# Performance work log

Measured on AMD Instinct MI355X. Metric: run time of the kernel, lower is better.

## Reference

```python
import jax, jax.numpy as jnp
import numpy as np

B, N, C, H, EXP = 8, 1024, 256, 8, 4
D = C // H
F = int(C * EXP * 2 / 3)  # 682, GLU hidden size
EPS = 1e-3  # keras LayerNormalization default


def layer_norm(x, g, b):
    m = jnp.mean(x, axis=-1, keepdims=True)
    v = jnp.mean(jnp.square(x - m), axis=-1, keepdims=True)
    return (x - m) * jax.lax.rsqrt(v + EPS) * g + b


def setup_inputs() -> dict:
    key = jax.random.key(0)
    ks = jax.random.split(key, 16)
    inputs = jax.random.normal(ks[0], (B, N, C), jnp.float32)
    # ragged padding mask: random valid lengths per batch element
    lengths = jax.random.randint(ks[1], (B,), N // 2, N + 1)
    valid = jnp.arange(N)[None, :] < lengths[:, None]          # [B,N]
    mask = valid[:, :, None] & valid[:, None, :]               # [B,N,N]
    interaction = jax.random.normal(ks[2], (B, N, N, H), jnp.float32)
    s = lambda k, sh, fan: jax.random.normal(k, sh, jnp.float32) / np.sqrt(fan)
    return {
        "inputs": inputs, "mask": mask, "interaction": interaction,
        "Wqkv": s(ks[3], (C, 3 * C), C), "bqkv": jnp.zeros((3 * C,), jnp.float32),
        "Wt1": s(ks[4], (H, H), H), "bt1": jnp.zeros((H,), jnp.float32),
        "Wt2": s(ks[5], (H, H), H), "bt2": jnp.zeros((H,), jnp.float32),
        "Wout": s(ks[6], (C, C), C), "bout": jnp.zeros((C,), jnp.float32),
        "ln1_g": jnp.ones((C,), jnp.float32), "ln1_b": jnp.zeros((C,), jnp.float32),
        "ln2_g": jnp.ones((C,), jnp.float32), "ln2_b": jnp.zeros((C,), jnp.float32),
        "gamma1": jnp.full((C,), 1e-5, jnp.float32),
        "gamma2": jnp.full((C,), 1e-5, jnp.float32),
        "W_wide": s(ks[7], (C, F), C), "W_gate": s(ks[8], (C, F), C),
        "W_down": s(ks[9], (F, C), F),
        "lnf_g": jnp.ones((F,), jnp.float32), "lnf_b": jnp.zeros((F,), jnp.float32),
    }


def reference(inputs, mask, interaction, Wqkv, bqkv, Wt1, bt1, Wt2, bt2,
              Wout, bout, ln1_g, ln1_b, ln2_g, ln2_b, gamma1, gamma2,
              W_wide, W_gate, W_down, lnf_g, lnf_b):
    # --- pre-norm talking-heads self-attention ---
    h = layer_norm(inputs, ln1_g, ln1_b)
    qkv = (h @ Wqkv + bqkv).reshape(B, N, 3, H, D)
    qkv = jnp.transpose(qkv, (2, 0, 3, 1, 4))                 # [3,B,H,N,D]
    q, k, v = qkv[0], qkv[1], qkv[2]
    scores = jnp.einsum('bhnd,bhmd->bhnm', q, k) / np.sqrt(D) # [B,H,N,N]
    # talking heads 1 (pre-softmax head mixing, with bias)
    scores = jnp.einsum('bhnm,hg->bgnm', scores, Wt1) + bt1[None, :, None, None]
    scores = scores + jnp.transpose(interaction, (0, 3, 1, 2))
    # keras Softmax(mask): add -1e9 to masked positions
    scores = jnp.where(mask[:, None, :, :], scores, scores - 1e9)
    attn = jax.nn.softmax(scores, axis=-1)                    # pure attention
    # talking heads 2 (post-softmax head mixing)
    attn2 = jnp.einsum('bhnm,hg->bgnm', attn, Wt2) + bt2[None, :, None, None]
    out = jnp.einsum('bhnm,bhmd->bhnd', attn2, v)
    out = jnp.transpose(out, (0, 2, 1, 3)).reshape(B, N, C)
    out = out @ Wout + bout
    x = inputs + gamma1 * out                                  # LayerScale residual
    # --- GLU FFN with inner LayerNorm ---
    h2 = layer_norm(x, ln2_g, ln2_b)
    f = jax.nn.gelu(h2 @ W_wide, approximate=False) * (h2 @ W_gate)
    f = layer_norm(f, lnf_g, lnf_b)
    f = f @ W_down
    x = x + gamma2 * f
    return x
```

## Files before the change

kernel.cpp:

```cpp
#include <hip/hip_runtime.h>
#include <hip/hip_bf16.h>
#include <math.h>

#define B_ 8
#define N_ 1024
#define C_ 256
#define H_ 8
#define D_ 32
#define F_ 682
#define FP_ 704
#define EPS_ 1e-3f

typedef const __hip_bfloat16* bf16cp;
typedef __hip_bfloat16 bf16;
typedef __attribute__((ext_vector_type(8))) short short8;
typedef __attribute__((ext_vector_type(4))) float f32x4;

__device__ __forceinline__ float b2f(bf16 v){ return __bfloat162float(v); }
__device__ __forceinline__ float us2f(unsigned int u){ return __uint_as_float(u << 16); }
__device__ __forceinline__ unsigned short f2bu(float f){
  unsigned int u = __float_as_uint(f);
  return (unsigned short)((u + 0x7FFFu + ((u >> 16) & 1u)) >> 16);
}

__device__ __forceinline__ float ldf(const void* p, size_t i, int bf){
  return bf ? b2f(((bf16cp)p)[i]) : ((const float*)p)[i];
}

struct Ptrs { const void* p[22]; };

__global__ __launch_bounds__(64) void k_sniffp(Ptrs ptrs, int* flags){
  int i = blockIdx.x;
  int lane = threadIdx.x;
  if (i == 1){ if (lane == 0) flags[1] = 0; return; }
  const int sizes[22] = {2097152, 8388608, 8388608, 196608, 768, 64, 8, 64, 8,
                         65536, 256, 256, 256, 256, 256, 256, 256,
                         174592, 174592, 174592, 682, 682};
  const unsigned short* u = (const unsigned short*)ptrs.p[i];
  int nu = sizes[i] < 64 ? sizes[i] : 64;
  unsigned short x = 0;
  if (lane < nu) x = u[lane];
  int predB = 0;
  if (lane < nu){
    float vb = us2f((unsigned int)x);
    float ab = fabsf(vb);
    predB = (!(vb == 0.0f) && (!(ab <= 1e3f) || ab < 1e-30f || vb != vb)) ? 1 : 0;
  }
  unsigned long long mB = __ballot(predB);
  int badB = __popcll(mB);
  unsigned long long mEven = __ballot(lane < nu && (lane & 1) == 0 && x != 0);
  unsigned long long mOdd  = __ballot(lane < nu && (lane & 1) == 1 && x != 0);
  int evenAllZero = (mEven == 0ull);
  int oddAny = (mOdd != 0ull);
  unsigned short xa = (unsigned short)__shfl((int)x, (lane * 2) & 63);
  unsigned short xb = (unsigned short)__shfl((int)x, (lane * 2 + 1) & 63);
  int predF = 0;
  if (lane < (nu >> 1)){
    unsigned int w = ((unsigned int)xa) | (((unsigned int)xb) << 16);
    float vf = __uint_as_float(w);
    float af = fabsf(vf);
    predF = (!(vf == 0.0f) && (!(af <= 1e3f) || af < 1e-30f || vf != vf)) ? 1 : 0;
  }
  int badF = __popcll(__ballot(predF));
  if (lane == 0){
    int bf;
    if (badB > badF) bf = 0;
    else if (badF > badB) bf = 1;
    else bf = (evenAllZero && oddAny) ? 0 : 1;
    flags[i] = bf;
  }
}

__global__ __launch_bounds__(256) void k_lengths(const unsigned char* mask, int* lengths){
  __shared__ int red[256];
  int b = blockIdx.x, t = threadIdx.x;
  unsigned char c0 = mask[0], c1 = mask[1];
  int mode;
  if (c0 == 0x80u) mode = 2;
  else if (c0 == 0u) mode = 3;
  else mode = (c1 != 0u) ? 0 : 1;
  int cnt = 0;
  for (int n = t; n < N_; n += 256){
    size_t idx = ((size_t)b*N_ + n)*N_ + n;
    int v;
    if (mode == 0)      v = (mask[idx] != 0);
    else if (mode == 1) v = (((const int*)mask)[idx] != 0);
    else if (mode == 2) v = (((const unsigned short*)mask)[idx] != 0);
    else                v = (((const float*)mask)[idx] != 0.0f);
    cnt += v;
  }
  red[t] = cnt; __syncthreads();
  for (int s = 128; s > 0; s >>= 1){ if (t < s) red[t] += red[t+s]; __syncthreads(); }
  if (t == 0) lengths[b] = red[0];
}

__global__ __launch_bounds__(256) void k_ln(const void* in, const int* flags, int in_mode,
                                            const void* g, int gi, const void* bia, int bi,
                                            void* out, int out_bf16, int Clen, int stride){
  __shared__ float red[256];
  int fin = (in_mode >= 0) ? flags[in_mode] : (in_mode == -2 ? 1 : 0);
  int fg = flags[gi], fb = flags[bi];
  int row = blockIdx.x, t = threadIdx.x;
  size_t base = (size_t)row * stride;
  float xs[3];
  int nv = (Clen + 255) >> 8;
  float s = 0.f;
  for (int i = 0; i < nv; i++){
    int c = t + (i << 8);
    float v = 0.f;
    if (c < Clen) v = ldf(in, base+c, fin);
    xs[i] = v; s += v;
  }
  red[t] = s; __syncthreads();
  for (int st = 128; st > 0; st >>= 1){ if (t < st) red[t] += red[t+st]; __syncthreads(); }
  float mean = red[0] / (float)Clen; __syncthreads();
  float s2 = 0.f;
  for (int i = 0; i < nv; i++){
    int c = t + (i << 8);
    if (c < Clen){ float d = xs[i] - mean; s2 += d*d; }
  }
  red[t] = s2; __syncthreads();
  for (int st = 128; st > 0; st >>= 1){ if (t < st) red[t] += red[t+st]; __syncthreads(); }
  float rstd = rsqrtf(red[0] / (float)Clen + EPS_);
  for (int i = 0; i < nv; i++){
    int c = t + (i << 8);
    if (c < Clen){
      float v = (xs[i]-mean)*rstd*ldf(g,c,fg) + ldf(bia,c,fb);
      if (out_bf16) ((bf16*)out)[base+c] = __float2bfloat16(v);
      else          ((float*)out)[base+c] = v;
    }
  }
}

__global__ __launch_bounds__(256) void k_prepw(Ptrs ptrs, const int* flags,
                                               unsigned short* wqkvT, unsigned short* woutT,
                                               unsigned short* wwideT, unsigned short* wgateT,
                                               unsigned short* wdownT){
  __shared__ unsigned short tile[32][33];
  int which = blockIdx.y;
  const void* src; unsigned short* dst; int f, Ksrc, Nsrc, Np, Kp;
  switch (which){
    case 0:  src = ptrs.p[3];  f = flags[3];  Ksrc = 256; Nsrc = 768; Np = 768; Kp = 256; dst = wqkvT; break;
    case 1:  src = ptrs.p[9];  f = flags[9];  Ksrc = 256; Nsrc = 256; Np = 256; Kp = 256; dst = woutT; break;
    case 2:  src = ptrs.p[17]; f = flags[17]; Ksrc = 256; Nsrc = F_;  Np = FP_; Kp = 256; dst = wwideT; break;
    case 3:  src = ptrs.p[18]; f = flags[18]; Ksrc = 256; Nsrc = F_;  Np = FP_; Kp = 256; dst = wgateT; break;
    default: src = ptrs.p[19]; f = flags[19]; Ksrc = F_;  Nsrc = 256; Np = 256; Kp = FP_; dst = wdownT; break;
  }
  int tilesN = (Np + 31) >> 5, tilesK = (Kp + 31) >> 5;
  int tid = blockIdx.x;
  if (tid >= tilesN * tilesK) return;
  int tn = tid % tilesN, tk = tid / tilesN;
  int n0 = tn << 5, k0 = tk << 5;
  int tx = threadIdx.x & 31, ty = threadIdx.x >> 5;
  #pragma unroll
  for (int i = 0; i < 4; i++){
    int k = k0 + ty + i*8, n = n0 + tx;
    float v = (k < Ksrc && n < Nsrc) ? ldf(src, (size_t)k*Nsrc + n, f) : 0.f;
    tile[ty + i*8][tx] = f2bu(v);
  }
  __syncthreads();
  #pragma unroll
  for (int i = 0; i < 4; i++){
    int n = n0 + ty + i*8, k = k0 + tx;
    if (n < Np && k < Kp) dst[(size_t)n*Kp + k] = tile[tx][ty + i*8];
  }
}

__global__ __launch_bounds__(256) void k_vt(const bf16* vb, unsigned short* vt){
  __shared__ unsigned short tile[32][34];
  int mt = blockIdx.x, bg = blockIdx.y;
  int tx = threadIdx.x & 31, ty = threadIdx.x >> 5;
  const unsigned short* vus = (const unsigned short*)vb;
  #pragma unroll
  for (int i = 0; i < 4; i++){
    int m = mt*32 + ty + i*8;
    tile[ty + i*8][tx] = vus[((size_t)bg*N_ + m)*D_ + tx];
  }
  __syncthreads();
  #pragma unroll
  for (int i = 0; i < 4; i++){
    int d = ty + i*8;
    vt[((size_t)bg*D_ + d)*N_ + mt*32 + tx] = tile[tx][d];
  }
}

__device__ __forceinline__ void gemm128_core(const unsigned short* A, const unsigned short* BT,
                                             int K, int m0, int n0,
                                             unsigned short* As, unsigned short* Bs,
                                             f32x4 (&acc)[4][4]){
  int t = threadIdx.x;
  int lane = t & 63, w = t >> 6, wr = w >> 1, wc = w & 1;
  int cl = lane & 15, cq = lane >> 4;
  int r0 = t >> 2, o0 = (t & 3) << 3;
  const unsigned short* Ap = A + (size_t)(m0 + r0) * K + o0;
  const unsigned short* Bp = BT + (size_t)(n0 + r0) * K + o0;
  for (int k0 = 0; k0 < K; k0 += 32){
    short8 a0 = *(const short8*)(Ap + k0);
    short8 a1 = *(const short8*)(Ap + (size_t)64*K + k0);
    short8 b0 = *(const short8*)(Bp + k0);
    short8 b1 = *(const short8*)(Bp + (size_t)64*K + k0);
    __syncthreads();
    *(short8*)(As + r0*40 + o0)      = a0;
    *(short8*)(As + (r0+64)*40 + o0) = a1;
    *(short8*)(Bs + r0*40 + o0)      = b0;
    *(short8*)(Bs + (r0+64)*40 + o0) = b1;
    __syncthreads();
    short8 af[4], bfr[4];
    #pragma unroll
    for (int i = 0; i < 4; i++){
      af[i]  = *(const short8*)(As + (wr*64 + i*16 + cl)*40 + cq*8);
      bfr[i] = *(const short8*)(Bs + (wc*64 + i*16 + cl)*40 + cq*8);
    }
    #pragma unroll
    for (int i = 0; i < 4; i++)
      #pragma unroll
      for (int j = 0; j < 4; j++)
        acc[i][j] = __builtin_amdgcn_mfma_f32_16x16x32_bf16(af[i], bfr[j], acc[i][j], 0, 0, 0);
  }
}

__global__ __launch_bounds__(256) void k_qkv(const bf16* Abuf, const unsigned short* WT,
                                             const void* bias, const int* flags,
                                             bf16* qb, bf16* kb, bf16* vb){
  __shared__ unsigned short As[128*40], Bs[128*40];
  int fb = flags[4];
  int m0 = blockIdx.x * 128, n0 = blockIdx.y * 128;
  f32x4 acc[4][4];
  #pragma unroll
  for (int i = 0; i < 4; i++)
    #pragma unroll
    for (int j = 0; j < 4; j++){ f32x4 z = {0.f,0.f,0.f,0.f}; acc[i][j] = z; }
  gemm128_core((const unsigned short*)Abuf, WT, C_, m0, n0, As, Bs, acc);
  int t = threadIdx.x, lane = t & 63, w = t >> 6, wr = w >> 1, wc = w & 1;
  int cl = lane & 15, cq = lane >> 4;
  #pragma unroll
  for (int j = 0; j < 4; j++){
    int n = n0 + wc*64 + j*16 + cl;
    float bv = ldf(bias, n, fb);
    int three = n >> 8, hh = (n >> 5) & 7, d = n & 31;
    bf16* dst = (three == 0) ? qb : ((three == 1) ? kb : vb);
    #pragma unroll
    for (int i = 0; i < 4; i++){
      #pragma unroll
      for (int r = 0; r < 4; r++){
        int m = m0 + wr*64 + i*16 + cq*4 + r;
        int bb = m >> 10, nn = m & 1023;
        dst[(((size_t)bb*H_ + hh)*N_ + nn)*D_ + d] = __float2bfloat16(acc[i][j][r] + bv);
      }
    }
  }
}

__global__ __launch_bounds__(256) void k_outproj(const bf16* Abuf, const unsigned short* WT,
                                                 const void* bias, const void* inputs,
                                                 const void* gamma1, const int* flags, float* xout){
  __shared__ unsigned short As[128*40], Bs[128*40];
  int fb = flags[10], fin = flags[0], fg = flags[15];
  int m0 = blockIdx.x * 128, n0 = blockIdx.y * 128;
  f32x4 acc[4][4];
  #pragma unroll
  for (int i = 0; i < 4; i++)
    #pragma unroll
    for (int j = 0; j < 4; j++){ f32x4 z = {0.f,0.f,0.f,0.f}; acc[i][j] = z; }
  gemm128_core((const unsigned short*)Abuf, WT, C_, m0, n0, As, Bs, acc);
  int t = threadIdx.x, lane = t & 63, w = t >> 6, wr = w >> 1, wc = w & 1;
  int cl = lane & 15, cq = lane >> 4;
  #pragma unroll
  for (int j = 0; j < 4; j++){
    int n = n0 + wc*64 + j*16 + cl;
    float bv = ldf(bias, n, fb);
    float gv = ldf(gamma1, n, fg);
    #pragma unroll
    for (int i = 0; i < 4; i++){
      #pragma unroll
      for (int r = 0; r < 4; r++){
        int m = m0 + wr*64 + i*16 + cq*4 + r;
        size_t idx = (size_t)m*C_ + n;
        xout[idx] = ldf(inputs, idx, fin) + gv * (acc[i][j][r] + bv);
      }
    }
  }
}

__device__ __forceinline__ float gelu_exact(float x){
  return 0.5f * x * (1.0f + erff(x * 0.70710678118654752f));
}

__global__ __launch_bounds__(256) void k_ffn1(const bf16* Abuf, const unsigned short* WwT,
                                              const unsigned short* WgT, bf16* fout){
  __shared__ unsigned short As[128*40], Bw[64*40], Bg[64*40];
  int m0 = blockIdx.x * 128, n0 = blockIdx.y * 64;
  int t = threadIdx.x, lane = t & 63, w = t >> 6, wr = w >> 1, wc = w & 1;
  int cl = lane & 15, cq = lane >> 4;
  int r0 = t >> 2, o0 = (t & 3) << 3;
  const unsigned short* A = (const unsigned short*)Abuf;
  f32x4 acc1[4][2], acc2[4][2];
  #pragma unroll
  for (int i = 0; i < 4; i++)
    #pragma unroll
    for (int j = 0; j < 2; j++){ f32x4 z = {0.f,0.f,0.f,0.f}; acc1[i][j] = z; acc2[i][j] = z; }
  const unsigned short* Ap = A + (size_t)(m0 + r0) * C_ + o0;
  const unsigned short* Bwp = WwT + (size_t)(n0 + r0) * C_ + o0;
  const unsigned short* Bgp = WgT + (size_t)(n0 + r0) * C_ + o0;
  for (int k0 = 0; k0 < C_; k0 += 32){
    short8 a0 = *(const short8*)(Ap + k0);
    short8 a1 = *(const short8*)(Ap + (size_t)64*C_ + k0);
    short8 b0, c0;
    if (r0 < 64){
      b0 = *(const short8*)(Bwp + k0);
      c0 = *(const short8*)(Bgp + k0);
    }
    __syncthreads();
    *(short8*)(As + r0*40 + o0)      = a0;
    *(short8*)(As + (r0+64)*40 + o0) = a1;
    if (r0 < 64){
      *(short8*)(Bw + r0*40 + o0) = b0;
      *(short8*)(Bg + r0*40 + o0) = c0;
    }
    __syncthreads();
    short8 af[4], bfr[2], cfr[2];
    #pragma unroll
    for (int i = 0; i < 4; i++)
      af[i] = *(const short8*)(As + (wr*64 + i*16 + cl)*40 + cq*8);
    #pragma unroll
    for (int j = 0; j < 2; j++){
      bfr[j] = *(const short8*)(Bw + (wc*32 + j*16 + cl)*40 + cq*8);
      cfr[j] = *(const short8*)(Bg + (wc*32 + j*16 + cl)*40 + cq*8);
    }
    #pragma unroll
    for (int i = 0; i < 4; i++)
      #pragma unroll
      for (int j = 0; j < 2; j++){
        acc1[i][j] = __builtin_amdgcn_mfma_f32_16x16x32_bf16(af[i], bfr[j], acc1[i][j], 0, 0, 0);
        acc2[i][j] = __builtin_amdgcn_mfma_f32_16x16x32_bf16(af[i], cfr[j], acc2[i][j], 0, 0, 0);
      }
  }
  #pragma unroll
  for (int j = 0; j < 2; j++){
    int n = n0 + wc*32 + j*16 + cl;
    #pragma unroll
    for (int i = 0; i < 4; i++){
      #pragma unroll
      for (int r = 0; r < 4; r++){
        int m = m0 + wr*64 + i*16 + cq*4 + r;
        float v = (n < F_) ? gelu_exact(acc1[i][j][r]) * acc2[i][j][r] : 0.f;
        fout[(size_t)m*FP_ + n] = __float2bfloat16(v);
      }
    }
  }
}

__global__ __launch_bounds__(256) void k_down(const bf16* Abuf, const unsigned short* WT,
                                              const float* xbuf, const void* gamma2,
                                              const int* flags, void* out){
  __shared__ unsigned short As[128*40], Bs[128*40];
  int fg = flags[16], fo = flags[0];
  int m0 = blockIdx.x * 128, n0 = blockIdx.y * 128;
  f32x4 acc[4][4];
  #pragma unroll
  for (int i = 0; i < 4; i++)
    #pragma unroll
    for (int j = 0; j < 4; j++){ f32x4 z = {0.f,0.f,0.f,0.f}; acc[i][j] = z; }
  gemm128_core((const unsigned short*)Abuf, WT, FP_, m0, n0, As, Bs, acc);
  int t = threadIdx.x, lane = t & 63, w = t >> 6, wr = w >> 1, wc = w & 1;
  int cl = lane & 15, cq = lane >> 4;
  #pragma unroll
  for (int j = 0; j < 4; j++){
    int n = n0 + wc*64 + j*16 + cl;
    float gv = ldf(gamma2, n, fg);
    #pragma unroll
    for (int i = 0; i < 4; i++){
      #pragma unroll
      for (int r = 0; r < 4; r++){
        int m = m0 + wr*64 + i*16 + cq*4 + r;
        size_t idx = (size_t)m*C_ + n;
        float val = xbuf[idx] + gv * acc[i][j][r];
        if (fo) ((bf16*)out)[idx] = __float2bfloat16(val);
        else    ((float*)out)[idx] = val;
      }
    }
  }
}

__global__ __launch_bounds__(256) void k_vsum(const bf16* vb, float* vsum){
  __shared__ float red[8][32];
  int bg = blockIdx.x;
  int t = threadIdx.x;
  int d = t & 31, mg = t >> 5;
  float s = 0.f;
  for (int m = mg*128; m < mg*128 + 128; m++)
    s += b2f(vb[((size_t)bg*N_ + m)*D_ + d]);
  red[mg][d] = s; __syncthreads();
  if (t < 32){
    float a = 0.f;
    #pragma unroll
    for (int i = 0; i < 8; i++) a += red[i][t];
    vsum[(size_t)bg*D_ + t] = a;
  }
}

__global__ __launch_bounds__(256) void k_passA(const bf16* qb, const bf16* kb,
                                               const void* Wt1, const void* bt1, const void* inter,
                                               const int* flags, const int* lengths,
                                               unsigned short* P, float* Lp){
  __shared__ float w1s[64], b1v[8];
  __shared__ unsigned short ps[4][8][640];
  __shared__ float swL[4][8][16];
  int fw1 = flags[5], fb1 = flags[6], fint = flags[2];
  int t = threadIdx.x;
  int ntile = blockIdx.x, b = blockIdx.y, z = blockIdx.z;
  int n0 = ntile * 16;
  int len = lengths[b];
  if (t < 64) w1s[t] = ldf(Wt1, t, fw1) * 0.17677669529663687f;
  if (t < 8)  b1v[t] = ldf(bt1, t, fb1);
  __syncthreads();
  int lane = t & 63, w = t >> 6;
  int c = lane & 15, q = lane >> 4;
  const unsigned short* qus = (const unsigned short*)qb;
  const unsigned short* kus = (const unsigned short*)kb;
  short8 qfrag[8];
  #pragma unroll
  for (int h = 0; h < 8; h++)
    qfrag[h] = *(const short8*)(qus + (((size_t)b*8 + h)*N_ + n0 + c)*D_ + q*8);
  float Lacc[8][4];
  #pragma unroll
  for (int g = 0; g < 8; g++)
    #pragma unroll
    for (int r = 0; r < 4; r++) Lacc[g][r] = 0.f;

  for (int ci = 0; ci < 4; ci++){
    int m0c = z*512 + w*128 + ci*32;
    #pragma unroll
    for (int mt = 0; mt < 2; mt++){
      int m0t = m0c + mt*16;
      f32x4 sfr[8];
      #pragma unroll
      for (int h = 0; h < 8; h++){
        short8 kf = *(const short8*)(kus + (((size_t)b*8 + h)*N_ + m0t + c)*D_ + q*8);
        f32x4 zz = {0.f,0.f,0.f,0.f};
        sfr[h] = __builtin_amdgcn_mfma_f32_16x16x32_bf16(qfrag[h], kf, zz, 0, 0, 0);
      }
      int m_g = m0t + c;
      bool mok = (m_g < len);
      #pragma unroll
      for (int r = 0; r < 4; r++){
        int n_l = q*4 + r, n_gg = n0 + n_l;
        size_t i8 = ((size_t)b*N_ + n_gg)*N_ + m_g;
        float ifl[8];
        if (fint){
          uint4 iv = *(const uint4*)((const unsigned short*)inter + i8*8);
          ifl[0]=us2f(iv.x&0xffffu); ifl[1]=us2f(iv.x>>16);
          ifl[2]=us2f(iv.y&0xffffu); ifl[3]=us2f(iv.y>>16);
          ifl[4]=us2f(iv.z&0xffffu); ifl[5]=us2f(iv.z>>16);
          ifl[6]=us2f(iv.w&0xffffu); ifl[7]=us2f(iv.w>>16);
        } else {
          const float* fp = (const float*)inter + i8*8;
          #pragma unroll
          for (int g = 0; g < 8; g++) ifl[g] = fp[g];
        }
        bool ok = (n_gg >= len) || mok;
        #pragma unroll
        for (int g = 0; g < 8; g++){
          float v = b1v[g] + ifl[g];
          #pragma unroll
          for (int h = 0; h < 8; h++) v += sfr[h][r] * w1s[h*8 + g];
          float e = ok ? __expf(v) : 0.f;
          Lacc[g][r] += e;
          ps[w][g][n_l*40 + mt*16 + c] = f2bu(e);
        }
      }
    }
    #pragma unroll
    for (int it = 0; it < 8; it++){
      int row = it*16 + (lane >> 2);
      int g = row >> 4, n = row & 15, chunk = lane & 3;
      short8 pv = *(const short8*)&ps[w][g][n*40 + chunk*8];
      *(short8*)(P + (((size_t)b*8 + g)*N_ + n0 + n)*N_ + m0c + chunk*8) = pv;
    }
  }
  #pragma unroll
  for (int g = 0; g < 8; g++)
    #pragma unroll
    for (int r = 0; r < 4; r++){
      float v = Lacc[g][r];
      v += __shfl_xor(v, 1); v += __shfl_xor(v, 2);
      v += __shfl_xor(v, 4); v += __shfl_xor(v, 8);
      Lacc[g][r] = v;
    }
  if (c == 0){
    #pragma unroll
    for (int g = 0; g < 8; g++)
      #pragma unroll
      for (int r = 0; r < 4; r++) swL[w][g][q*4 + r] = Lacc[g][r];
  }
  __syncthreads();
  if (t < 128){
    int g = t >> 4, nl = t & 15;
    float Lf = swL[0][g][nl] + swL[1][g][nl] + swL[2][g][nl] + swL[3][g][nl];
    Lp[(((size_t)b*8 + g)*N_ + n0 + nl)*2 + z] = Lf;
  }
}

__global__ __launch_bounds__(256) void k_passB(const unsigned short* P, const unsigned short* vt,
                                               const void* Wt2, const void* bt2,
                                               const int* flags, const float* Lp,
                                               const float* vsum, bf16* aobuf){
  __shared__ float w2s[64], b2v[8];
  __shared__ float rLs[8][16];
  __shared__ float vsumS[4][32];
  __shared__ float osum[4][528];
  int fw2 = flags[7], fb2 = flags[8];
  int t = threadIdx.x;
  int ntile = blockIdx.x, b = blockIdx.y, zh = blockIdx.z;
  int n0 = ntile * 16;
  if (t < 64) w2s[t] = ldf(Wt2, t, fw2);
  if (t < 8)  b2v[t] = ldf(bt2, t, fb2);
  if (t < 128){
    int g = t >> 4, nl = t & 15;
    const float* lp = Lp + (((size_t)b*8 + g)*N_ + n0 + nl)*2;
    rLs[g][nl] = 1.0f / (lp[0] + lp[1]);
  }
  if (t >= 128 && t < 256){
    int e = t - 128;
    int g2 = e >> 5, d = e & 31;
    vsumS[g2][d] = vsum[((size_t)b*8 + zh*4 + g2)*D_ + d];
  }
  __syncthreads();
  int lane = t & 63, w = t >> 6;
  int c = lane & 15, q = lane >> 4;
  float rL[8];
  #pragma unroll
  for (int g = 0; g < 8; g++) rL[g] = rLs[g][c];
  float w2r[8][4];
  #pragma unroll
  for (int g = 0; g < 8; g++)
    #pragma unroll
    for (int j = 0; j < 4; j++) w2r[g][j] = w2s[g*8 + zh*4 + j];
  f32x4 acc[4][2];
  #pragma unroll
  for (int gg = 0; gg < 4; gg++){ f32x4 z = {0.f,0.f,0.f,0.f}; acc[gg][0] = z; acc[gg][1] = z; }

  for (int ci = 0; ci < 8; ci++){
    int m0c = w*256 + ci*32;
    short8 pf[8];
    #pragma unroll
    for (int g = 0; g < 8; g++)
      pf[g] = *(const short8*)(P + (((size_t)b*8 + g)*N_ + n0 + c)*N_ + m0c + q*8);
    float a2[4][8];
    #pragma unroll
    for (int gg = 0; gg < 4; gg++)
      #pragma unroll
      for (int j = 0; j < 8; j++) a2[gg][j] = 0.f;
    #pragma unroll
    for (int j = 0; j < 8; j++){
      #pragma unroll
      for (int g = 0; g < 8; g++){
        float png = us2f((unsigned int)(unsigned short)pf[g][j]) * rL[g];
        a2[0][j] += png * w2r[g][0];
        a2[1][j] += png * w2r[g][1];
        a2[2][j] += png * w2r[g][2];
        a2[3][j] += png * w2r[g][3];
      }
    }
    #pragma unroll
    for (int gg = 0; gg < 4; gg++){
      short8 af;
      #pragma unroll
      for (int j = 0; j < 8; j++) af[j] = (short)f2bu(a2[gg][j]);
      int ggg = zh*4 + gg;
      short8 bf0 = *(const short8*)(vt + (((size_t)b*8 + ggg)*D_ + c)*N_ + m0c + q*8);
      short8 bf1 = *(const short8*)(vt + (((size_t)b*8 + ggg)*D_ + 16 + c)*N_ + m0c + q*8);
      acc[gg][0] = __builtin_amdgcn_mfma_f32_16x16x32_bf16(af, bf0, acc[gg][0], 0, 0, 0);
      acc[gg][1] = __builtin_amdgcn_mfma_f32_16x16x32_bf16(af, bf1, acc[gg][1], 0, 0, 0);
    }
  }
  for (int gg = 0; gg < 4; gg++){
    #pragma unroll
    for (int dt = 0; dt < 2; dt++)
      #pragma unroll
      for (int r = 0; r < 4; r++)
        osum[w][(q*4 + r)*33 + dt*16 + c] = acc[gg][dt][r];
    __syncthreads();
    int ggg = zh*4 + gg;
    #pragma unroll
    for (int e = t; e < 512; e += 256){
      int nl = e >> 5, d = e & 31;
      float val = osum[0][nl*33 + d] + osum[1][nl*33 + d]
                + osum[2][nl*33 + d] + osum[3][nl*33 + d]
                + b2v[ggg] * vsumS[gg][d];
      aobuf[((size_t)b*N_ + n0 + nl)*C_ + ggg*D_ + d] = __float2bfloat16(val);
    }
    __syncthreads();
  }
}

extern "C" void kernel_launch(void* const* d_in, const int* in_sizes, int n_in,
                              void* d_out, int out_size, void* d_ws, size_t ws_size,
                              hipStream_t stream) {
  Ptrs ptrs;
  for (int i = 0; i < 22; i++) ptrs.p[i] = d_in[i];
  const unsigned char* mask = (const unsigned char*)d_in[1];

  char* ws = (char*)d_ws;
  size_t o = 0;
  size_t o_flags = o; o += 256;
  size_t o_len   = o; o += 256;
  size_t o_L     = o; o += (size_t)B_*H_*N_*2*4;
  size_t o_vsum  = o; o += (size_t)B_*H_*D_*4;
  size_t o_h     = o; o += (size_t)B_*N_*C_*2;
  size_t o_q     = o; o += (size_t)B_*N_*C_*2;
  size_t o_k     = o; o += (size_t)B_*N_*C_*2;
  size_t o_v     = o; o += (size_t)B_*N_*C_*2;
  size_t o_vt    = o; o += (size_t)B_*N_*C_*2;
  size_t o_ao    = o; o += (size_t)B_*N_*C_*2;
  size_t o_x     = o; o += (size_t)B_*N_*C_*4;
  size_t o_f     = o; o += (size_t)B_*N_*FP_*2;
  size_t o_wq    = o; o += (size_t)768*256*2;
  size_t o_wo    = o; o += (size_t)256*256*2;
  size_t o_ww    = o; o += (size_t)FP_*256*2;
  size_t o_wg    = o; o += (size_t)FP_*256*2;
  size_t o_wd    = o; o += (size_t)256*FP_*2;
  size_t o_P     = o; o += (size_t)B_*H_*N_*N_*2;

  int*    flags   = (int*)(ws + o_flags);
  int*    lengths = (int*)(ws + o_len);
  float*  Lp      = (float*)(ws + o_L);
  float*  vsum    = (float*)(ws + o_vsum);
  bf16*   hbuf    = (bf16*)(ws + o_h);
  bf16*   qbuf    = (bf16*)(ws + o_q);
  bf16*   kbuf    = (bf16*)(ws + o_k);
  bf16*   vbuf    = (bf16*)(ws + o_v);
  unsigned short* vtbuf = (unsigned short*)(ws + o_vt);
  bf16*   aobuf   = (bf16*)(ws + o_ao);
  float*  xbuf    = (float*)(ws + o_x);
  bf16*   fbuf    = (bf16*)(ws + o_f);
  unsigned short* wqkvT  = (unsigned short*)(ws + o_wq);
  unsigned short* woutT  = (unsigned short*)(ws + o_wo);
  unsigned short* wwideT = (unsigned short*)(ws + o_ww);
  unsigned short* wgateT = (unsigned short*)(ws + o_wg);
  unsigned short* wdownT = (unsigned short*)(ws + o_wd);
  unsigned short* Pbuf   = (unsigned short*)(ws + o_P);

  k_sniffp<<<22, 64, 0, stream>>>(ptrs, flags);
  k_prepw<<<dim3(192, 5), 256, 0, stream>>>(ptrs, flags, wqkvT, woutT, wwideT, wgateT, wdownT);
  k_lengths<<<8, 256, 0, stream>>>(mask, lengths);
  k_ln<<<B_*N_, 256, 0, stream>>>(d_in[0], flags, 0, d_in[11], 11, d_in[12], 12, hbuf, 1, C_, C_);
  k_qkv<<<dim3(64, 6), 256, 0, stream>>>(hbuf, wqkvT, d_in[4], flags, qbuf, kbuf, vbuf);
  k_vt<<<dim3(32, 64), 256, 0, stream>>>(vbuf, vtbuf);
  k_vsum<<<64, 256, 0, stream>>>(vbuf, vsum);
  k_passA<<<dim3(64, 8, 2), 256, 0, stream>>>(qbuf, kbuf, d_in[5], d_in[6], d_in[2],
                                              flags, lengths, Pbuf, Lp);
  k_passB<<<dim3(64, 8, 2), 256, 0, stream>>>(Pbuf, vtbuf, d_in[7], d_in[8],
                                              flags, Lp, vsum, aobuf);
  k_outproj<<<dim3(64, 2), 256, 0, stream>>>(aobuf, woutT, d_in[10], d_in[0], d_in[15], flags, xbuf);
  k_ln<<<B_*N_, 256, 0, stream>>>(xbuf, flags, -1, d_in[13], 13, d_in[14], 14, hbuf, 1, C_, C_);
  k_ffn1<<<dim3(64, 11), 256, 0, stream>>>(hbuf, wwideT, wgateT, fbuf);
  k_ln<<<B_*N_, 256, 0, stream>>>(fbuf, flags, -2, d_in[20], 20, d_in[21], 21, fbuf, 1, F_, FP_);
  k_down<<<dim3(64, 2), 256, 0, stream>>>(fbuf, wdownT, xbuf, d_in[16], flags, d_out);
}
```

Baseline: 851.1 us.

## Fold talking-heads pre-softmax mix into Q so MFMA computes mixed scores directly

Adds a kernel that premultiplies Q by the Wt1 head-mixing weights, producing one mixed Q per output head over the full 256-wide channel. passA can then compute mixed scores with a K=256 MFMA contraction instead of eight per-head MFMAs followed by a scalar 8x8 mix per element. Q and K are now stored flat, Q tiles are staged in XOR-swizzled shared memory, the z-split over keys is removed, and P is written directly without the shared staging buffer. passB loads P in two groups of four heads to cut register pressure. The cost is an extra kernel and a 32 MB qmix buffer. The P stores become scattered 2-byte writes and the grid has half as many blocks.

```diff
diff --git a/kernel.cpp b/kernel.cpp
--- a/kernel.cpp
+++ b/kernel.cpp
@@ -221,7 +221,7 @@
 
 __global__ __launch_bounds__(256) void k_qkv(const bf16* Abuf, const unsigned short* WT,
                                              const void* bias, const int* flags,
-                                             bf16* qb, bf16* kb, bf16* vb){
+                                             bf16* qflat, bf16* kflat, bf16* vb){
   __shared__ unsigned short As[128*40], Bs[128*40];
   int fb = flags[4];
   int m0 = blockIdx.x * 128, n0 = blockIdx.y * 128;
@@ -238,16 +238,41 @@
     int n = n0 + wc*64 + j*16 + cl;
     float bv = ldf(bias, n, fb);
     int three = n >> 8, hh = (n >> 5) & 7, d = n & 31;
-    bf16* dst = (three == 0) ? qb : ((three == 1) ? kb : vb);
     #pragma unroll
     for (int i = 0; i < 4; i++){
       #pragma unroll
       for (int r = 0; r < 4; r++){
         int m = m0 + wr*64 + i*16 + cq*4 + r;
         int bb = m >> 10, nn = m & 1023;
-        dst[(((size_t)bb*H_ + hh)*N_ + nn)*D_ + d] = __float2bfloat16(acc[i][j][r] + bv);
-      }
-    }
+        bf16 val = __float2bfloat16(acc[i][j][r] + bv);
+        if (three == 0)      qflat[((size_t)bb*N_ + nn)*C_ + hh*32 + d] = val;
+        else if (three == 1) kflat[((size_t)bb*N_ + nn)*C_ + hh*32 + d] = val;
+        else                 vb[(((size_t)bb*H_ + hh)*N_ + nn)*D_ + d] = val;
+      }
+    }
+  }
+}
+
+__global__ __launch_bounds__(256) void k_qmix(const bf16* qflat, const void* Wt1, const int* flags,
+                                              unsigned short* qmix){
+  __shared__ float w1s[64];
+  int t = threadIdx.x;
+  if (t < 64) w1s[t] = ldf(Wt1, t, flags[5]) * 0.17677669529663687f;
+  __syncthreads();
+  int ntile = blockIdx.x, b = blockIdx.y;
+  const unsigned short* qus = (const unsigned short*)qflat;
+  for (int it = 0; it < 16; it++){
+    int flat = it*256 + t;
+    int g = flat >> 9, nl = (flat >> 5) & 15, c8 = flat & 31;
+    int h = c8 >> 2;
+    int nn = ntile*16 + nl;
+    short8 qv = *(const short8*)(qus + ((size_t)b*N_ + nn)*C_ + c8*8);
+    float wv = w1s[h*8 + g];
+    short8 ov;
+    #pragma unroll
+    for (int j = 0; j < 8; j++)
+      ov[j] = (short)f2bu(us2f((unsigned int)(unsigned short)qv[j]) * wv);
+    *(short8*)(qmix + (((size_t)b*8 + g)*N_ + nn)*C_ + c8*8) = ov;
   }
 }
 
@@ -399,83 +424,83 @@
   }
 }
 
-__global__ __launch_bounds__(256) void k_passA(const bf16* qb, const bf16* kb,
-                                               const void* Wt1, const void* bt1, const void* inter,
+__global__ __launch_bounds__(256) void k_passA(const unsigned short* qmix, const unsigned short* kflat,
+                                               const void* bt1, const void* inter,
                                                const int* flags, const int* lengths,
                                                unsigned short* P, float* Lp){
-  __shared__ float w1s[64], b1v[8];
-  __shared__ unsigned short ps[4][8][640];
+  __shared__ unsigned short qls[128*256];
   __shared__ float swL[4][8][16];
-  int fw1 = flags[5], fb1 = flags[6], fint = flags[2];
+  int fb1 = flags[6], fint = flags[2];
   int t = threadIdx.x;
-  int ntile = blockIdx.x, b = blockIdx.y, z = blockIdx.z;
+  int ntile = blockIdx.x, b = blockIdx.y;
   int n0 = ntile * 16;
   int len = lengths[b];
-  if (t < 64) w1s[t] = ldf(Wt1, t, fw1) * 0.17677669529663687f;
-  if (t < 8)  b1v[t] = ldf(bt1, t, fb1);
+  float b1r[8];
+  #pragma unroll
+  for (int g = 0; g < 8; g++) b1r[g] = ldf(bt1, g, fb1);
+  for (int it = 0; it < 16; it++){
+    int flat = it*256 + t;
+    int row = flat >> 5, ch = flat & 31;
+    int g = row >> 4, nl = row & 15;
+    short8 v = *(const short8*)(qmix + (((size_t)b*8 + g)*N_ + n0 + nl)*C_ + ch*8);
+    unsigned int off = (unsigned)row*512u + (unsigned)ch*16u;
+    off ^= (unsigned)((row & 7) << 4);
+    *(short8*)((char*)qls + off) = v;
+  }
   __syncthreads();
   int lane = t & 63, w = t >> 6;
   int c = lane & 15, q = lane >> 4;
-  const unsigned short* qus = (const unsigned short*)qb;
-  const unsigned short* kus = (const unsigned short*)kb;
-  short8 qfrag[8];
-  #pragma unroll
-  for (int h = 0; h < 8; h++)
-    qfrag[h] = *(const short8*)(qus + (((size_t)b*8 + h)*N_ + n0 + c)*D_ + q*8);
   float Lacc[8][4];
   #pragma unroll
   for (int g = 0; g < 8; g++)
     #pragma unroll
     for (int r = 0; r < 4; r++) Lacc[g][r] = 0.f;
 
-  for (int ci = 0; ci < 4; ci++){
-    int m0c = z*512 + w*128 + ci*32;
-    #pragma unroll
-    for (int mt = 0; mt < 2; mt++){
-      int m0t = m0c + mt*16;
-      f32x4 sfr[8];
-      #pragma unroll
-      for (int h = 0; h < 8; h++){
-        short8 kf = *(const short8*)(kus + (((size_t)b*8 + h)*N_ + m0t + c)*D_ + q*8);
-        f32x4 zz = {0.f,0.f,0.f,0.f};
-        sfr[h] = __builtin_amdgcn_mfma_f32_16x16x32_bf16(qfrag[h], kf, zz, 0, 0, 0);
-      }
-      int m_g = m0t + c;
-      bool mok = (m_g < len);
-      #pragma unroll
-      for (int r = 0; r < 4; r++){
-        int n_l = q*4 + r, n_gg = n0 + n_l;
-        size_t i8 = ((size_t)b*N_ + n_gg)*N_ + m_g;
-        float ifl[8];
-        if (fint){
-          uint4 iv = *(const uint4*)((const unsigned short*)inter + i8*8);
-          ifl[0]=us2f(iv.x&0xffffu); ifl[1]=us2f(iv.x>>16);
-          ifl[2]=us2f(iv.y&0xffffu); ifl[3]=us2f(iv.y>>16);
-          ifl[4]=us2f(iv.z&0xffffu); ifl[5]=us2f(iv.z>>16);
-          ifl[6]=us2f(iv.w&0xffffu); ifl[7]=us2f(iv.w>>16);
-        } else {
-          const float* fp = (const float*)inter + i8*8;
-          #pragma unroll
-          for (int g = 0; g < 8; g++) ifl[g] = fp[g];
-        }
-        bool ok = (n_gg >= len) || mok;
-        #pragma unroll
-        for (int g = 0; g < 8; g++){
-          float v = b1v[g] + ifl[g];
-          #pragma unroll
-          for (int h = 0; h < 8; h++) v += sfr[h][r] * w1s[h*8 + g];
-          float e = ok ? __expf(v) : 0.f;
-          Lacc[g][r] += e;
-          ps[w][g][n_l*40 + mt*16 + c] = f2bu(e);
-        }
-      }
-    }
-    #pragma unroll
-    for (int it = 0; it < 8; it++){
-      int row = it*16 + (lane >> 2);
-      int g = row >> 4, n = row & 15, chunk = lane & 3;
-      short8 pv = *(const short8*)&ps[w][g][n*40 + chunk*8];
-      *(short8*)(P + (((size_t)b*8 + g)*N_ + n0 + n)*N_ + m0c + chunk*8) = pv;
+  for (int mt = 0; mt < 16; mt++){
+    int m0t = w*256 + mt*16;
+    f32x4 acc[8];
+    #pragma unroll
+    for (int g = 0; g < 8; g++){ f32x4 z = {0.f,0.f,0.f,0.f}; acc[g] = z; }
+    const unsigned short* kfp = kflat + ((size_t)b*N_ + m0t + c)*C_ + q*8;
+    #pragma unroll
+    for (int kc = 0; kc < 8; kc++){
+      short8 kf = *(const short8*)(kfp + kc*32);
+      #pragma unroll
+      for (int g = 0; g < 8; g++){
+        unsigned int off = ((unsigned)(g*16 + c)*512u + (unsigned)(kc*64 + q*16)) ^ (unsigned)((c & 7) << 4);
+        short8 qm = *(const short8*)((const char*)qls + off);
+        acc[g] = __builtin_amdgcn_mfma_f32_16x16x32_bf16(qm, kf, acc[g], 0, 0, 0);
+      }
+    }
+    int m_g = m0t + c;
+    bool mok = (m_g < len);
+    #pragma unroll
+    for (int r = 0; r < 4; r++){
+      int n_gg = n0 + q*4 + r;
+      size_t i8 = ((size_t)b*N_ + n_gg)*N_ + m_g;
+      float ifl[8];
+      if (fint){
+        uint4 iv = *(const uint4*)((const unsigned short*)inter + i8*8);
+        ifl[0]=us2f(iv.x&0xffffu); ifl[1]=us2f(iv.x>>16);
+        ifl[2]=us2f(iv.y&0xffffu); ifl[3]=us2f(iv.y>>16);
+        ifl[4]=us2f(iv.z&0xffffu); ifl[5]=us2f(iv.z>>16);
+        ifl[6]=us2f(iv.w&0xffffu); ifl[7]=us2f(iv.w>>16);
+      } else {
+        const float* fp = (const float*)inter + i8*8;
+        float4 fa = *(const float4*)fp;
+        float4 fb2 = *(const float4*)(fp + 4);
+        ifl[0]=fa.x; ifl[1]=fa.y; ifl[2]=fa.z; ifl[3]=fa.w;
+        ifl[4]=fb2.x; ifl[5]=fb2.y; ifl[6]=fb2.z; ifl[7]=fb2.w;
+      }
+      bool ok = (n_gg >= len) || mok;
+      size_t pbase = (((size_t)b*8)*N_ + n_gg)*N_ + m_g;
+      #pragma unroll
+      for (int g = 0; g < 8; g++){
+        float v = acc[g][r] + b1r[g] + ifl[g];
+        float e = ok ? __expf(v) : 0.f;
+        Lacc[g][r] += e;
+        P[pbase + (size_t)g*N_*N_] = f2bu(e);
+      }
     }
   }
   #pragma unroll
@@ -497,7 +522,7 @@
   if (t < 128){
     int g = t >> 4, nl = t & 15;
     float Lf = swL[0][g][nl] + swL[1][g][nl] + swL[2][g][nl] + swL[3][g][nl];
-    Lp[(((size_t)b*8 + g)*N_ + n0 + nl)*2 + z] = Lf;
+    Lp[((size_t)b*8 + g)*N_ + n0 + nl] = Lf;
   }
 }
 
@@ -517,8 +542,7 @@
   if (t < 8)  b2v[t] = ldf(bt2, t, fb2);
   if (t < 128){
     int g = t >> 4, nl = t & 15;
-    const float* lp = Lp + (((size_t)b*8 + g)*N_ + n0 + nl)*2;
-    rLs[g][nl] = 1.0f / (lp[0] + lp[1]);
+    rLs[g][nl] = 1.0f / Lp[((size_t)b*8 + g)*N_ + n0 + nl];
   }
   if (t >= 128 && t < 256){
     int e = t - 128;
@@ -535,31 +559,35 @@
   #pragma unroll
   for (int g = 0; g < 8; g++)
     #pragma unroll
-    for (int j = 0; j < 4; j++) w2r[g][j] = w2s[g*8 + zh*4 + j];
+    for (int j = 0; j < 4; j++)
+      w2r[g][j] = __builtin_amdgcn_readfirstlane(w2s[g*8 + zh*4 + j]);
   f32x4 acc[4][2];
   #pragma unroll
   for (int gg = 0; gg < 4; gg++){ f32x4 z = {0.f,0.f,0.f,0.f}; acc[gg][0] = z; acc[gg][1] = z; }
 
   for (int ci = 0; ci < 8; ci++){
     int m0c = w*256 + ci*32;
-    short8 pf[8];
-    #pragma unroll
-    for (int g = 0; g < 8; g++)
-      pf[g] = *(const short8*)(P + (((size_t)b*8 + g)*N_ + n0 + c)*N_ + m0c + q*8);
     float a2[4][8];
     #pragma unroll
     for (int gg = 0; gg < 4; gg++)
       #pragma unroll
       for (int j = 0; j < 8; j++) a2[gg][j] = 0.f;
     #pragma unroll
-    for (int j = 0; j < 8; j++){
-      #pragma unroll
-      for (int g = 0; g < 8; g++){
-        float png = us2f((unsigned int)(unsigned short)pf[g][j]) * rL[g];
-        a2[0][j] += png * w2r[g][0];
-        a2[1][j] += png * w2r[g][1];
-        a2[2][j] += png * w2r[g][2];
-        a2[3][j] += png * w2r[g][3];
+    for (int g4 = 0; g4 < 2; g4++){
+      short8 pf[4];
+      #pragma unroll
+      for (int g = 0; g < 4; g++)
+        pf[g] = *(const short8*)(P + (((size_t)b*8 + g4*4 + g)*N_ + n0 + c)*N_ + m0c + q*8);
+      #pragma unroll
+      for (int j = 0; j < 8; j++){
+        #pragma unroll
+        for (int g = 0; g < 4; g++){
+          float png = us2f((unsigned int)(unsigned short)pf[g][j]) * rL[g4*4 + g];
+          a2[0][j] += png * w2r[g4*4 + g][0];
+          a2[1][j] += png * w2r[g4*4 + g][1];
+          a2[2][j] += png * w2r[g4*4 + g][2];
+          a2[3][j] += png * w2r[g4*4 + g][3];
+        }
       }
     }
     #pragma unroll
@@ -605,11 +633,11 @@
   size_t o = 0;
   size_t o_flags = o; o += 256;
   size_t o_len   = o; o += 256;
-  size_t o_L     = o; o += (size_t)B_*H_*N_*2*4;
+  size_t o_L     = o; o += (size_t)B_*H_*N_*4;
   size_t o_vsum  = o; o += (size_t)B_*H_*D_*4;
   size_t o_h     = o; o += (size_t)B_*N_*C_*2;
   size_t o_q     = o; o += (size_t)B_*N_*C_*2;
-  size_t o_k     = o; o += (size_t)B_*N_*C_*2;
+  size_t o_kf    = o; o += (size_t)B_*N_*C_*2;
   size_t o_v     = o; o += (size_t)B_*N_*C_*2;
   size_t o_vt    = o; o += (size_t)B_*N_*C_*2;
   size_t o_ao    = o; o += (size_t)B_*N_*C_*2;
@@ -620,6 +648,7 @@
   size_t o_ww    = o; o += (size_t)FP_*256*2;
   size_t o_wg    = o; o += (size_t)FP_*256*2;
   size_t o_wd    = o; o += (size_t)256*FP_*2;
+  size_t o_qm    = o; o += (size_t)B_*H_*N_*C_*2;
   size_t o_P     = o; o += (size_t)B_*H_*N_*N_*2;
 
   int*    flags   = (int*)(ws + o_flags);
@@ -627,8 +656,8 @@
   float*  Lp      = (float*)(ws + o_L);
   float*  vsum    = (float*)(ws + o_vsum);
   bf16*   hbuf    = (bf16*)(ws + o_h);
-  bf16*   qbuf    = (bf16*)(ws + o_q);
-  bf16*   kbuf    = (bf16*)(ws + o_k);
+  bf16*   qflat   = (bf16*)(ws + o_q);
+  bf16*   kflat   = (bf16*)(ws + o_kf);
   bf16*   vbuf    = (bf16*)(ws + o_v);
   unsigned short* vtbuf = (unsigned short*)(ws + o_vt);
   bf16*   aobuf   = (bf16*)(ws + o_ao);
@@ -639,17 +668,19 @@
   unsigned short* wwideT = (unsigned short*)(ws + o_ww);
   unsigned short* wgateT = (unsigned short*)(ws + o_wg);
   unsigned short* wdownT = (unsigned short*)(ws + o_wd);
+  unsigned short* qmix   = (unsigned short*)(ws + o_qm);
   unsigned short* Pbuf   = (unsigned short*)(ws + o_P);
 
   k_sniffp<<<22, 64, 0, stream>>>(ptrs, flags);
   k_prepw<<<dim3(192, 5), 256, 0, stream>>>(ptrs, flags, wqkvT, woutT, wwideT, wgateT, wdownT);
   k_lengths<<<8, 256, 0, stream>>>(mask, lengths);
   k_ln<<<B_*N_, 256, 0, stream>>>(d_in[0], flags, 0, d_in[11], 11, d_in[12], 12, hbuf, 1, C_, C_);
-  k_qkv<<<dim3(64, 6), 256, 0, stream>>>(hbuf, wqkvT, d_in[4], flags, qbuf, kbuf, vbuf);
+  k_qkv<<<dim3(64, 6), 256, 0, stream>>>(hbuf, wqkvT, d_in[4], flags, qflat, kflat, vbuf);
+  k_qmix<<<dim3(64, 8), 256, 0, stream>>>(qflat, d_in[5], flags, qmix);
   k_vt<<<dim3(32, 64), 256, 0, stream>>>(vbuf, vtbuf);
   k_vsum<<<64, 256, 0, stream>>>(vbuf, vsum);
-  k_passA<<<dim3(64, 8, 2), 256, 0, stream>>>(qbuf, kbuf, d_in[5], d_in[6], d_in[2],
-                                              flags, lengths, Pbuf, Lp);
+  k_passA<<<dim3(64, 8), 256, 0, stream>>>(qmix, (const unsigned short*)kflat, d_in[6], d_in[2],
+                                           flags, lengths, Pbuf, Lp);
   k_passB<<<dim3(64, 8, 2), 256, 0, stream>>>(Pbuf, vtbuf, d_in[7], d_in[8],
                                               flags, Lp, vsum, aobuf);
   k_outproj<<<dim3(64, 2), 256, 0, stream>>>(aobuf, woutT, d_in[10], d_in[0], d_in[15], flags, xbuf);
```

After: 878.2 us. +3.2%, slower.
